# Kernel tuning notes

Hardware: AMD Instinct MI355X
Metric: run time of the kernel (lower is better)

The kernel has to match this reference:

```python
import jax, jax.numpy as jnp
import numpy as np

C_M, C_Z, C = 256, 128, 32
LN_EPS = 1e-5


def setup_inputs() -> dict:
    key = jax.random.key(0)
    ks = jax.random.split(key, 9)
    S, R = 128, 384  # N_seq, N_res
    m = jax.random.normal(ks[0], (S, R, C_M), dtype=jnp.float32)
    ln_g = jnp.ones((C_M,), jnp.float32)
    ln_b = jnp.zeros((C_M,), jnp.float32)
    w1 = jax.random.normal(ks[1], (C_M, C), jnp.float32) / np.sqrt(C_M)
    b1 = jnp.zeros((C,), jnp.float32)
    w2 = jax.random.normal(ks[2], (C_M, C), jnp.float32) / np.sqrt(C_M)
    b2 = jnp.zeros((C,), jnp.float32)
    w_out = jax.random.normal(ks[3], (C * C, C_Z), jnp.float32) / np.sqrt(C * C)
    b_out = jnp.zeros((C_Z,), jnp.float32)
    return {"m": m, "ln_g": ln_g, "ln_b": ln_b, "w1": w1, "b1": b1,
            "w2": w2, "b2": b2, "w_out": w_out, "b_out": b_out}


def reference(m, ln_g, ln_b, w1, b1, w2, b2, w_out, b_out):
    S, R, _ = m.shape
    # LayerNorm over c_m
    mu = jnp.mean(m, axis=-1, keepdims=True)
    var = jnp.var(m, axis=-1, keepdims=True)
    mn = (m - mu) * jax.lax.rsqrt(var + LN_EPS) * ln_g + ln_b
    a = mn @ w1 + b1  # (S, R, c)
    b = mn @ w2 + b2  # (S, R, c)
    # outer product summed over N_seq: out[i,j,x,y] = sum_s a[s,i,x] b[s,j,y]
    o = jnp.einsum('six,sjy->ijxy', a, b)  # (R, R, c, c)
    o = o.reshape(R, R, C * C) @ w_out + b_out  # (R, R, c_z)
    return o / S
```

## Files before the change

kernel.cpp:

```cpp
#include <hip/hip_runtime.h>
#include <hip/hip_bf16.h>

#define R_RES 384
#define S_SEQ 128
#define CM 256
#define CC 32
#define CZ 128

typedef __attribute__((ext_vector_type(8))) short bf16x8;
typedef __attribute__((ext_vector_type(4))) float f32x4;
typedef __attribute__((ext_vector_type(16))) float f32x16;
typedef __attribute__((ext_vector_type(4))) int i32x4;

__device__ __forceinline__ short tobf16(float f) {
    union { __hip_bfloat16 h; short s; } u;
    u.h = __float2bfloat16(f);
    return u.s;
}

__global__ void k_transpose_wout(const float* __restrict__ w_out, short* __restrict__ wbTf) {
    __shared__ float t[64][65];
    int k0 = blockIdx.x * 64;
    int z0 = blockIdx.y * 64;
    int tid = threadIdx.x;
    int c = tid & 63, rg = tid >> 6;
#pragma unroll
    for (int rr = 0; rr < 16; ++rr) {
        int kk = rg * 16 + rr;
        t[kk][c] = w_out[(size_t)(k0 + kk) * CZ + z0 + c];
    }
    __syncthreads();
#pragma unroll
    for (int l = 0; l < 2; ++l) {
        int id = l * 256 + tid;
        int f = id >> 6;
        int ksl = f >> 1, fzl = f & 1;
        int ln = id & 63;
        int zl = fzl * 32 + (ln & 31);
        int kl = ksl * 16 + (ln >> 5) * 8;
        bf16x8 pk;
#pragma unroll
        for (int j = 0; j < 8; ++j) pk[j] = tobf16(t[kl + j][zl]);
        size_t fz = blockIdx.y * 2 + fzl;
        size_t ks16 = blockIdx.x * 4 + ksl;
        *(bf16x8*)(wbTf + ((fz * 64 + ks16) * 64 + ln) * 8) = pk;
    }
}

__global__ void k_pack_w12(const float* __restrict__ w1, const float* __restrict__ w2,
                           short* __restrict__ wcT) {
    int idx = blockIdx.x * 256 + threadIdx.x;
    int k = idx >> 6, n = idx & 63;
    float v = (n < 32) ? w1[k * CC + n] : w2[k * CC + (n - 32)];
    wcT[n * CM + k] = tobf16(v);
}

__global__ __launch_bounds__(256) void k_ln_proj(
    const float* __restrict__ M, const float* __restrict__ ln_g, const float* __restrict__ ln_b,
    const float* __restrict__ b1, const float* __restrict__ b2,
    const short* __restrict__ wcT, short* __restrict__ aTf, short* __restrict__ bTf) {
    __shared__ short mnb[64 * 256];
    __shared__ short ab_s[2][32 * 72];
    int r = blockIdx.x >> 1;
    int s0 = (blockIdx.x & 1) * 64;
    int tid = threadIdx.x, lane = tid & 63, w = tid >> 6;
    int g = lane >> 4, r16 = lane & 15;
    float4 gv = *(const float4*)(ln_g + lane * 4);
    float4 bv = *(const float4*)(ln_b + lane * 4);
    for (int it = 0; it < 16; ++it) {
        int sl = it * 4 + w;
        float4 v = *(const float4*)(M + ((size_t)(s0 + sl) * R_RES + r) * CM + lane * 4);
        float sum = v.x + v.y + v.z + v.w;
        float sq = v.x * v.x + v.y * v.y + v.z * v.z + v.w * v.w;
#pragma unroll
        for (int off = 32; off; off >>= 1) {
            sum += __shfl_xor(sum, off);
            sq  += __shfl_xor(sq, off);
        }
        float mu = sum * (1.0f / 256.0f);
        float var = sq * (1.0f / 256.0f) - mu * mu;
        float rstd = rsqrtf(var + 1e-5f);
        short4 mnp;
        mnp.x = tobf16((v.x - mu) * rstd * gv.x + bv.x);
        mnp.y = tobf16((v.y - mu) * rstd * gv.y + bv.y);
        mnp.z = tobf16((v.z - mu) * rstd * gv.z + bv.z);
        mnp.w = tobf16((v.w - mu) * rstd * gv.w + bv.w);
        int byte = sl * 512 + lane * 8;
        byte ^= ((sl & 7) << 4);
        *(short4*)((char*)mnb + byte) = mnp;
    }
    __syncthreads();
    f32x4 acc[4] = {{0,0,0,0},{0,0,0,0},{0,0,0,0},{0,0,0,0}};
    int srow = w * 16 + r16;
#pragma unroll
    for (int ks = 0; ks < 8; ++ks) {
        int byte = srow * 512 + ks * 64 + g * 16;
        byte ^= ((srow & 7) << 4);
        bf16x8 af = *(const bf16x8*)((const char*)mnb + byte);
#pragma unroll
        for (int nt = 0; nt < 4; ++nt) {
            bf16x8 bf = *(const bf16x8*)(wcT + (nt * 16 + r16) * CM + ks * 32 + g * 8);
            acc[nt] = __builtin_amdgcn_mfma_f32_16x16x32_bf16(af, bf, acc[nt], 0, 0, 0);
        }
    }
#pragma unroll
    for (int nt = 0; nt < 4; ++nt) {
        int n = nt * 16 + r16;
        int x = n & 31, sel = n >> 5;
        float bias = sel ? b2[x] : b1[x];
#pragma unroll
        for (int rr = 0; rr < 4; ++rr) {
            int sl = w * 16 + g * 4 + rr;
            ab_s[sel][x * 72 + sl] = tobf16(acc[nt][rr] + bias);
        }
    }
    __syncthreads();
    int piece = tid >> 6;
    int fl = piece >> 1, kl = piece & 1;
    int ln = tid & 63;
    int x = fl * 16 + (ln & 15);
    int s_loc = kl * 32 + (ln >> 4) * 8;
    i32x4 va = *(const i32x4*)((const char*)ab_s[0] + (x * 72 + s_loc) * 2);
    i32x4 vb = *(const i32x4*)((const char*)ab_s[1] + (x * 72 + s_loc) * 2);
    size_t off = ((((size_t)r * 2 + fl) * 4 + (s0 >> 5) + kl) * 64 + ln) * 16;
    *(i32x4*)((char*)aTf + off) = va;
    *(i32x4*)((char*)bTf + off) = vb;
}

__global__ __launch_bounds__(1024, 4) void k_opm(
    const short* __restrict__ aTf, const short* __restrict__ bTf,
    const short* __restrict__ wbTf, const float* __restrict__ b_out,
    float* __restrict__ out) {
    __shared__ __align__(16) char smem[131072];
    int tid = threadIdx.x, lane = tid & 63, w = tid >> 6;
    int g = lane >> 4, r16 = lane & 15;
    int l32 = lane & 31, h = lane >> 5;
    int wm = w & 3, wn = w >> 2;
    int bj = blockIdx.x, bi = blockIdx.y;

    const char* gA = (const char*)aTf + (size_t)bi * 65536;
    const char* gB = (const char*)bTf + (size_t)bj * 65536;
#pragma unroll
    for (int it = 0; it < 4; ++it) {
        int q = it * 16384 + tid * 16;
        __builtin_amdgcn_global_load_lds(
            (const __attribute__((address_space(1))) void*)(gA + q),
            (__attribute__((address_space(3))) void*)(smem + q), 16, 0, 0);
        __builtin_amdgcn_global_load_lds(
            (const __attribute__((address_space(1))) void*)(gB + q),
            (__attribute__((address_space(3))) void*)(smem + 65536 + q), 16, 0, 0);
    }
    __syncthreads();

    f32x4 acc[4][4] = {};
#pragma unroll
    for (int ks = 0; ks < 4; ++ks) {
        bf16x8 bf[4], af[4];
#pragma unroll
        for (int ni = 0; ni < 4; ++ni)
            bf[ni] = *(const bf16x8*)(smem + 65536 + (((wn * 4 + ni) * 4 + ks) * 64 + lane) * 16);
#pragma unroll
        for (int mi = 0; mi < 4; ++mi)
            af[mi] = *(const bf16x8*)(smem + (((wm * 4 + mi) * 4 + ks) * 64 + lane) * 16);
        __builtin_amdgcn_s_setprio(1);
#pragma unroll
        for (int mi = 0; mi < 4; ++mi)
#pragma unroll
            for (int ni = 0; ni < 4; ++ni)
                acc[mi][ni] = __builtin_amdgcn_mfma_f32_16x16x32_bf16(bf[ni], af[mi], acc[mi][ni], 0, 0, 0);
        __builtin_amdgcn_s_setprio(0);
    }
    __syncthreads();

#pragma unroll
    for (int mi = 0; mi < 4; ++mi)
#pragma unroll
        for (int ni = 0; ni < 4; ++ni) {
            int m = wm * 64 + mi * 16 + r16;
            int nb = wn * 64 + ni * 16 + g * 4;
            int i = m >> 5, x = m & 31;
            int j = nb >> 5, y0 = nb & 31;
            int p = i * 8 + j;
            int byte = (p * 2048 + x * 64 + y0 * 2) ^ (((p & 7) ^ (x & 7)) << 4);
            short4 pk;
            pk.x = tobf16(acc[mi][ni][0]);
            pk.y = tobf16(acc[mi][ni][1]);
            pk.z = tobf16(acc[mi][ni][2]);
            pk.w = tobf16(acc[mi][ni][3]);
            *(short4*)(smem + byte) = pk;
        }
    __syncthreads();

    int kh = w & 1, zq = (w >> 1) & 3, pd = w >> 3;
    f32x16 c2a = {0,0,0,0,0,0,0,0,0,0,0,0,0,0,0,0};
    f32x16 c2b = {0,0,0,0,0,0,0,0,0,0,0,0,0,0,0,0};
    const short* wbase = wbTf + (size_t)((zq * 64 + kh * 32) * 64) * 8;
    int pbase = pd * 32 + l32;
#pragma unroll 8
    for (int ks = 0; ks < 32; ++ks) {
        int x = kh * 16 + (ks >> 1);
        int byte = (pbase * 2048 + kh * 1024 + ks * 32 + h * 16)
                   ^ ((((l32 & 7) ^ (x & 7))) << 4);
        bf16x8 a2f = *(const bf16x8*)(smem + byte);
        bf16x8 wbf = *(const bf16x8*)(wbase + (ks * 64 + lane) * 8);
        if (ks & 1) c2b = __builtin_amdgcn_mfma_f32_32x32x16_bf16(a2f, wbf, c2b, 0, 0, 0);
        else        c2a = __builtin_amdgcn_mfma_f32_32x32x16_bf16(a2f, wbf, c2a, 0, 0, 0);
    }
    f32x16 c2 = c2a + c2b;
    __syncthreads();

#pragma unroll
    for (int q = 0; q < 4; ++q)
#pragma unroll
        for (int rr = 0; rr < 4; ++rr) {
            int prow = pd * 32 + q * 8 + h * 4 + rr;
            int zz = zq * 32 + l32;
            int byte = (kh * 32768 + prow * 512 + zz * 4) ^ ((prow & 1) << 4);
            *(float*)(smem + byte) = c2[q * 4 + rr];
        }
    __syncthreads();

    {
        int p = tid >> 4;
        int zo = (tid & 15) * 8;
        int sw = (p & 1) << 4;
        int base = p * 512 + zo * 4;
        f32x4 u0 = *(const f32x4*)(smem + ((base) ^ sw));
        f32x4 u1 = *(const f32x4*)(smem + ((base + 16) ^ sw));
        f32x4 v0 = *(const f32x4*)(smem + ((base + 32768) ^ sw));
        f32x4 v1 = *(const f32x4*)(smem + ((base + 16 + 32768) ^ sw));
        float4 bo0 = *(const float4*)(b_out + zo);
        float4 bo1 = *(const float4*)(b_out + zo + 4);
        f32x4 r0, r1;
        r0[0] = (u0[0] + v0[0] + bo0.x) * (1.0f / 128.0f);
        r0[1] = (u0[1] + v0[1] + bo0.y) * (1.0f / 128.0f);
        r0[2] = (u0[2] + v0[2] + bo0.z) * (1.0f / 128.0f);
        r0[3] = (u0[3] + v0[3] + bo0.w) * (1.0f / 128.0f);
        r1[0] = (u1[0] + v1[0] + bo1.x) * (1.0f / 128.0f);
        r1[1] = (u1[1] + v1[1] + bo1.y) * (1.0f / 128.0f);
        r1[2] = (u1[2] + v1[2] + bo1.z) * (1.0f / 128.0f);
        r1[3] = (u1[3] + v1[3] + bo1.w) * (1.0f / 128.0f);
        int ig = bi * 8 + (p >> 3);
        int jg = bj * 8 + (p & 7);
        float* po = out + ((size_t)ig * R_RES + jg) * CZ + zo;
        *(f32x4*)(po) = r0;
        *(f32x4*)(po + 4) = r1;
    }
}

extern "C" void kernel_launch(void* const* d_in, const int* in_sizes, int n_in,
                              void* d_out, int out_size, void* d_ws, size_t ws_size,
                              hipStream_t stream) {
    const float* M     = (const float*)d_in[0];
    const float* ln_g  = (const float*)d_in[1];
    const float* ln_b  = (const float*)d_in[2];
    const float* w1    = (const float*)d_in[3];
    const float* b1    = (const float*)d_in[4];
    const float* w2    = (const float*)d_in[5];
    const float* b2    = (const float*)d_in[6];
    const float* w_out = (const float*)d_in[7];
    const float* b_out = (const float*)d_in[8];
    float* out = (float*)d_out;

    short* aTf  = (short*)d_ws;
    short* bTf  = aTf + 12288 * 128;
    short* wbTf = bTf + 12288 * 128;
    short* wcT  = wbTf + 128 * 1024;

    k_transpose_wout<<<dim3(16, 2), 256, 0, stream>>>(w_out, wbTf);
    k_pack_w12<<<64, 256, 0, stream>>>(w1, w2, wcT);
    k_ln_proj<<<768, 256, 0, stream>>>(M, ln_g, ln_b, b1, b2, wcT, aTf, bTf);
    k_opm<<<dim3(48, 48), 1024, 0, stream>>>(aTf, bTf, wbTf, b_out, out);
}
```

Before: 143.6 us.

## Retile outer-product kernel to 6x4 residue tiles with 512 threads and smaller LDS

The main kernel now computes a 6x4 residue-pair tile per block with 512 threads, where it previously used 8x8 with 1024 threads. LDS drops from 128KB to 48KB so more blocks can be resident per CU. Only the B operand is staged in LDS; the A fragments are read directly from global memory. The second GEMM is restructured to 16x16x32 MFMAs with register double-buffering of the w_out fragments, which needs a matching change to the w_out packing layout. Barriers are replaced with explicit lgkmcnt waits. The trade-off is more blocks and more redundant global reads of A and w_out per output.

```diff
diff --git a/kernel.cpp b/kernel.cpp
--- a/kernel.cpp
+++ b/kernel.cpp
@@ -9,13 +9,18 @@
 
 typedef __attribute__((ext_vector_type(8))) short bf16x8;
 typedef __attribute__((ext_vector_type(4))) float f32x4;
-typedef __attribute__((ext_vector_type(16))) float f32x16;
 typedef __attribute__((ext_vector_type(4))) int i32x4;
 
 __device__ __forceinline__ short tobf16(float f) {
     union { __hip_bfloat16 h; short s; } u;
     u.h = __float2bfloat16(f);
     return u.s;
+}
+
+__device__ __forceinline__ void lgkm_barrier() {
+    asm volatile("s_waitcnt lgkmcnt(0)" ::: "memory");
+    __builtin_amdgcn_s_barrier();
+    __builtin_amdgcn_sched_barrier(0);
 }
 
 __global__ void k_transpose_wout(const float* __restrict__ w_out, short* __restrict__ wbTf) {
@@ -34,16 +39,16 @@
     for (int l = 0; l < 2; ++l) {
         int id = l * 256 + tid;
         int f = id >> 6;
-        int ksl = f >> 1, fzl = f & 1;
+        int z16l = f >> 1, k32l = f & 1;
         int ln = id & 63;
-        int zl = fzl * 32 + (ln & 31);
-        int kl = ksl * 16 + (ln >> 5) * 8;
+        int zl = z16l * 16 + (ln & 15);
+        int kl = k32l * 32 + (ln >> 4) * 8;
         bf16x8 pk;
 #pragma unroll
         for (int j = 0; j < 8; ++j) pk[j] = tobf16(t[kl + j][zl]);
-        size_t fz = blockIdx.y * 2 + fzl;
-        size_t ks16 = blockIdx.x * 4 + ksl;
-        *(bf16x8*)(wbTf + ((fz * 64 + ks16) * 64 + ln) * 8) = pk;
+        int z16 = blockIdx.y * 4 + z16l;
+        int k32 = blockIdx.x * 2 + k32l;
+        *(bf16x8*)(wbTf + ((size_t)(z16 * 32 + k32) * 64 + ln) * 8) = pk;
     }
 }
 
@@ -127,60 +132,58 @@
     *(i32x4*)((char*)bTf + off) = vb;
 }
 
-__global__ __launch_bounds__(1024, 4) void k_opm(
+__global__ __launch_bounds__(512, 6) void k_opm(
     const short* __restrict__ aTf, const short* __restrict__ bTf,
     const short* __restrict__ wbTf, const float* __restrict__ b_out,
     float* __restrict__ out) {
-    __shared__ __align__(16) char smem[131072];
+    __shared__ __align__(16) char smem[49152];
     int tid = threadIdx.x, lane = tid & 63, w = tid >> 6;
     int g = lane >> 4, r16 = lane & 15;
-    int l32 = lane & 31, h = lane >> 5;
-    int wm = w & 3, wn = w >> 2;
+    int wm = w >> 1, wn = w & 1;
+    int kh = w & 1, zq = w >> 1;
     int bj = blockIdx.x, bi = blockIdx.y;
 
-    const char* gA = (const char*)aTf + (size_t)bi * 65536;
-    const char* gB = (const char*)bTf + (size_t)bj * 65536;
-#pragma unroll
-    for (int it = 0; it < 4; ++it) {
-        int q = it * 16384 + tid * 16;
+    const char* gB = (const char*)bTf + (size_t)bj * 32768;
+#pragma unroll
+    for (int q = 0; q < 4; ++q)
         __builtin_amdgcn_global_load_lds(
-            (const __attribute__((address_space(1))) void*)(gA + q),
-            (__attribute__((address_space(3))) void*)(smem + q), 16, 0, 0);
-        __builtin_amdgcn_global_load_lds(
-            (const __attribute__((address_space(1))) void*)(gB + q),
-            (__attribute__((address_space(3))) void*)(smem + 65536 + q), 16, 0, 0);
-    }
-    __syncthreads();
-
-    f32x4 acc[4][4] = {};
+            (const __attribute__((address_space(1))) void*)(gB + q * 8192 + tid * 16),
+            (__attribute__((address_space(3))) void*)(smem + q * 8192 + tid * 16), 16, 0, 0);
+    const char* gA = (const char*)aTf + (size_t)bi * 49152;
+    asm volatile("s_waitcnt vmcnt(0)" ::: "memory");
+    __syncthreads();
+
+    f32x4 acc[3][4] = {};
 #pragma unroll
     for (int ks = 0; ks < 4; ++ks) {
-        bf16x8 bf[4], af[4];
-#pragma unroll
-        for (int ni = 0; ni < 4; ++ni)
-            bf[ni] = *(const bf16x8*)(smem + 65536 + (((wn * 4 + ni) * 4 + ks) * 64 + lane) * 16);
-#pragma unroll
-        for (int mi = 0; mi < 4; ++mi)
-            af[mi] = *(const bf16x8*)(smem + (((wm * 4 + mi) * 4 + ks) * 64 + lane) * 16);
-        __builtin_amdgcn_s_setprio(1);
-#pragma unroll
-        for (int mi = 0; mi < 4; ++mi)
-#pragma unroll
-            for (int ni = 0; ni < 4; ++ni)
-                acc[mi][ni] = __builtin_amdgcn_mfma_f32_16x16x32_bf16(bf[ni], af[mi], acc[mi][ni], 0, 0, 0);
-        __builtin_amdgcn_s_setprio(0);
-    }
-    __syncthreads();
-
-#pragma unroll
-    for (int mi = 0; mi < 4; ++mi)
+        bf16x8 af[3];
+#pragma unroll
+        for (int mi = 0; mi < 3; ++mi)
+            af[mi] = *(const bf16x8*)(gA + ((wm * 3 + mi) * 4 + ks) * 1024 + lane * 16);
+#pragma unroll
+        for (int half = 0; half < 2; ++half) {
+            bf16x8 bf0 = *(const bf16x8*)(smem + (((wn * 4 + half * 2 + 0) * 4 + ks) * 64 + lane) * 16);
+            bf16x8 bf1 = *(const bf16x8*)(smem + (((wn * 4 + half * 2 + 1) * 4 + ks) * 64 + lane) * 16);
+            __builtin_amdgcn_s_setprio(1);
+#pragma unroll
+            for (int mi = 0; mi < 3; ++mi) {
+                acc[mi][half * 2 + 0] = __builtin_amdgcn_mfma_f32_16x16x32_bf16(bf0, af[mi], acc[mi][half * 2 + 0], 0, 0, 0);
+                acc[mi][half * 2 + 1] = __builtin_amdgcn_mfma_f32_16x16x32_bf16(bf1, af[mi], acc[mi][half * 2 + 1], 0, 0, 0);
+            }
+            __builtin_amdgcn_s_setprio(0);
+        }
+    }
+    lgkm_barrier();
+
+#pragma unroll
+    for (int mi = 0; mi < 3; ++mi)
 #pragma unroll
         for (int ni = 0; ni < 4; ++ni) {
-            int m = wm * 64 + mi * 16 + r16;
-            int nb = wn * 64 + ni * 16 + g * 4;
-            int i = m >> 5, x = m & 31;
-            int j = nb >> 5, y0 = nb & 31;
-            int p = i * 8 + j;
+            int fm = wm * 3 + mi;
+            int i = fm >> 1, x = (fm & 1) * 16 + r16;
+            int j = wn * 2 + (ni >> 1);
+            int y0 = (ni & 1) * 16 + g * 4;
+            int p = i * 4 + j;
             int byte = (p * 2048 + x * 64 + y0 * 2) ^ (((p & 7) ^ (x & 7)) << 4);
             short4 pk;
             pk.x = tobf16(acc[mi][ni][0]);
@@ -189,46 +192,61 @@
             pk.w = tobf16(acc[mi][ni][3]);
             *(short4*)(smem + byte) = pk;
         }
-    __syncthreads();
-
-    int kh = w & 1, zq = (w >> 1) & 3, pd = w >> 3;
-    f32x16 c2a = {0,0,0,0,0,0,0,0,0,0,0,0,0,0,0,0};
-    f32x16 c2b = {0,0,0,0,0,0,0,0,0,0,0,0,0,0,0,0};
-    const short* wbase = wbTf + (size_t)((zq * 64 + kh * 32) * 64) * 8;
-    int pbase = pd * 32 + l32;
-#pragma unroll 8
-    for (int ks = 0; ks < 32; ++ks) {
-        int x = kh * 16 + (ks >> 1);
-        int byte = (pbase * 2048 + kh * 1024 + ks * 32 + h * 16)
-                   ^ ((((l32 & 7) ^ (x & 7))) << 4);
-        bf16x8 a2f = *(const bf16x8*)(smem + byte);
-        bf16x8 wbf = *(const bf16x8*)(wbase + (ks * 64 + lane) * 8);
-        if (ks & 1) c2b = __builtin_amdgcn_mfma_f32_32x32x16_bf16(a2f, wbf, c2b, 0, 0, 0);
-        else        c2a = __builtin_amdgcn_mfma_f32_32x32x16_bf16(a2f, wbf, c2a, 0, 0, 0);
-    }
-    f32x16 c2 = c2a + c2b;
-    __syncthreads();
-
-#pragma unroll
-    for (int q = 0; q < 4; ++q)
-#pragma unroll
-        for (int rr = 0; rr < 4; ++rr) {
-            int prow = pd * 32 + q * 8 + h * 4 + rr;
-            int zz = zq * 32 + l32;
-            int byte = (kh * 32768 + prow * 512 + zz * 4) ^ ((prow & 1) << 4);
-            *(float*)(smem + byte) = c2[q * 4 + rr];
-        }
-    __syncthreads();
+
+    bf16x8 wcur0 = *(const bf16x8*)(wbTf + (((size_t)(zq * 2 + 0) * 32 + kh * 16 + 0) * 64 + lane) * 8);
+    bf16x8 wcur1 = *(const bf16x8*)(wbTf + (((size_t)(zq * 2 + 1) * 32 + kh * 16 + 0) * 64 + lane) * 8);
+    lgkm_barrier();
+
+    f32x4 c0 = {0,0,0,0}, c1 = {0,0,0,0}, c2 = {0,0,0,0}, c3 = {0,0,0,0};
+#pragma unroll
+    for (int ks2 = 0; ks2 < 16; ++ks2) {
+        bf16x8 wn0, wn1;
+        if (ks2 < 15) {
+            wn0 = *(const bf16x8*)(wbTf + (((size_t)(zq * 2 + 0) * 32 + kh * 16 + ks2 + 1) * 64 + lane) * 8);
+            wn1 = *(const bf16x8*)(wbTf + (((size_t)(zq * 2 + 1) * 32 + kh * 16 + ks2 + 1) * 64 + lane) * 8);
+        }
+        int x = kh * 16 + ks2;
+        bf16x8 a2f0 = *(const bf16x8*)(smem + ((r16 * 2048 + x * 64 + g * 16)
+                      ^ ((((r16 & 7) ^ (x & 7))) << 4)));
+        bf16x8 a2f1 = *(const bf16x8*)(smem + (((8 + r16) * 2048 + x * 64 + g * 16)
+                      ^ (((((8 + r16) & 7) ^ (x & 7))) << 4)));
+        __builtin_amdgcn_s_setprio(1);
+        c0 = __builtin_amdgcn_mfma_f32_16x16x32_bf16(wcur0, a2f0, c0, 0, 0, 0);
+        c1 = __builtin_amdgcn_mfma_f32_16x16x32_bf16(wcur1, a2f0, c1, 0, 0, 0);
+        c2 = __builtin_amdgcn_mfma_f32_16x16x32_bf16(wcur0, a2f1, c2, 0, 0, 0);
+        c3 = __builtin_amdgcn_mfma_f32_16x16x32_bf16(wcur1, a2f1, c3, 0, 0, 0);
+        __builtin_amdgcn_s_setprio(0);
+        if (ks2 < 15) { wcur0 = wn0; wcur1 = wn1; }
+    }
+    lgkm_barrier();
 
     {
+        int zb0 = zq * 32 + g * 4;
+        int zb1 = zq * 32 + 16 + g * 4;
+        int p0 = r16;
+        int b00 = (24576 + kh * 12288 + p0 * 512 + zb0 * 4) ^ ((p0 & 7) << 4);
+        int b01 = (24576 + kh * 12288 + p0 * 512 + zb1 * 4) ^ ((p0 & 7) << 4);
+        *(f32x4*)(smem + b00) = c0;
+        *(f32x4*)(smem + b01) = c1;
+        if (r16 >= 8) {
+            int p1 = 8 + r16;
+            int b10 = (24576 + kh * 12288 + p1 * 512 + zb0 * 4) ^ ((p1 & 7) << 4);
+            int b11 = (24576 + kh * 12288 + p1 * 512 + zb1 * 4) ^ ((p1 & 7) << 4);
+            *(f32x4*)(smem + b10) = c2;
+            *(f32x4*)(smem + b11) = c3;
+        }
+    }
+    lgkm_barrier();
+
+    if (tid < 384) {
         int p = tid >> 4;
         int zo = (tid & 15) * 8;
-        int sw = (p & 1) << 4;
-        int base = p * 512 + zo * 4;
+        int sw = (p & 7) << 4;
+        int base = 24576 + p * 512 + zo * 4;
         f32x4 u0 = *(const f32x4*)(smem + ((base) ^ sw));
         f32x4 u1 = *(const f32x4*)(smem + ((base + 16) ^ sw));
-        f32x4 v0 = *(const f32x4*)(smem + ((base + 32768) ^ sw));
-        f32x4 v1 = *(const f32x4*)(smem + ((base + 16 + 32768) ^ sw));
+        f32x4 v0 = *(const f32x4*)(smem + ((base + 12288) ^ sw));
+        f32x4 v1 = *(const f32x4*)(smem + ((base + 16 + 12288) ^ sw));
         float4 bo0 = *(const float4*)(b_out + zo);
         float4 bo1 = *(const float4*)(b_out + zo + 4);
         f32x4 r0, r1;
@@ -240,8 +258,8 @@
         r1[1] = (u1[1] + v1[1] + bo1.y) * (1.0f / 128.0f);
         r1[2] = (u1[2] + v1[2] + bo1.z) * (1.0f / 128.0f);
         r1[3] = (u1[3] + v1[3] + bo1.w) * (1.0f / 128.0f);
-        int ig = bi * 8 + (p >> 3);
-        int jg = bj * 8 + (p & 7);
+        int ig = bi * 6 + (p >> 2);
+        int jg = bj * 4 + (p & 3);
         float* po = out + ((size_t)ig * R_RES + jg) * CZ + zo;
         *(f32x4*)(po) = r0;
         *(f32x4*)(po + 4) = r1;
@@ -270,5 +288,5 @@
     k_transpose_wout<<<dim3(16, 2), 256, 0, stream>>>(w_out, wbTf);
     k_pack_w12<<<64, 256, 0, stream>>>(w1, w2, wcT);
     k_ln_proj<<<768, 256, 0, stream>>>(M, ln_g, ln_b, b1, b2, wcT, aTf, bTf);
-    k_opm<<<dim3(48, 48), 1024, 0, stream>>>(aTf, bTf, wbTf, b_out, out);
-}
+    k_opm<<<dim3(96, 64), 512, 0, stream>>>(aTf, bTf, wbTf, b_out, out);
+}
```

After: 182.5 us. 1.27x slower.
